# Kernel tuning notes

Hardware: AMD Instinct MI355X
Metric: run time of the kernel (lower is better)

Reference implementation:

```python
import jax, jax.numpy as jnp
import numpy as np

R = 100        # voxel grid resolution per axis
N = 200000     # number of active (non-empty) voxels
K = 3          # kernel size
CIN = 64
COUT = 64
NOFF = K ** 3 - 1  # 26 non-center offsets


def _build_maps():
    # Mirrors mapping_cuda: per kernel offset, find (input_row, output_row) pairs
    # such that coords[input] == coords[output] + offset (submanifold conv,
    # output coords == input coords).
    rng = np.random.default_rng(0)
    lin = rng.choice(R ** 3, size=N, replace=False)
    coords = np.stack(np.unravel_index(lin, (R, R, R)), axis=1)  # [N,3]
    lut = np.full(R ** 3, -1, dtype=np.int64)
    lut[lin] = np.arange(N)
    offs = [(dx, dy, dz) for dx in (-1, 0, 1) for dy in (-1, 0, 1)
            for dz in (-1, 0, 1) if (dx, dy, dz) != (0, 0, 0)]
    ins, outs = [], []
    for d in offs:
        tgt = coords - np.asarray(d)              # output coord receiving input i
        valid = np.all((tgt >= 0) & (tgt < R), axis=1)
        idx_i = np.nonzero(valid)[0]
        tlin = np.ravel_multi_index(tgt[valid].T, (R, R, R))
        j = lut[tlin]
        hit = j >= 0
        ins.append(idx_i[hit].astype(np.int32))
        outs.append(j[hit].astype(np.int32))
    P = max(len(a) for a in ins)
    imap = np.full((NOFF, P), -1, dtype=np.int32)
    omap = np.full((NOFF, P), -1, dtype=np.int32)
    for k, (a, b) in enumerate(zip(ins, outs)):
        imap[k, :len(a)] = a
        omap[k, :len(b)] = b
    return jnp.asarray(imap), jnp.asarray(omap)


def setup_inputs() -> dict:
    key = jax.random.key(0)
    kf, kw = jax.random.split(key)
    feats = jax.random.normal(kf, (N, CIN), dtype=jnp.float32)
    # reset_parameters: uniform(-stdv, stdv), stdv = 1/sqrt(out_channels * K^3)
    stdv = 1.0 / float(np.sqrt(COUT * K ** 3))
    kernel = jax.random.uniform(kw, (K ** 3, CIN, COUT), dtype=jnp.float32,
                                minval=-stdv, maxval=stdv)
    imap, omap = _build_maps()
    return {"feats": feats, "kernel": kernel, "imap": imap, "omap": omap}


def reference(feats, kernel, imap, omap):
    # Submanifold sparse 3D conv: gather -> per-offset GEMM -> scatter-add.
    K3 = kernel.shape[0]
    c = K3 // 2  # center offset: identity neighbor map
    w_nc = jnp.concatenate([kernel[:c], kernel[c + 1:]], axis=0)  # [26,Cin,Cout]
    mask = imap >= 0                                   # [26,P]
    gath = feats[jnp.where(mask, imap, 0)] * mask[..., None]   # [26,P,Cin]
    y = jnp.einsum('kpc,kco->kpo', gath, w_nc)         # [26,P,Cout]
    out = feats @ kernel[c]                            # center contribution [N,Cout]
    oi = jnp.where(mask, omap, 0).reshape(-1)          # masked rows add zeros at row 0
    out = out.at[oi].add(y.reshape(-1, y.shape[-1]))
    return out
```

## Files before the change

### kernel.cpp

```cpp
#include <hip/hip_runtime.h>


#define CIN 64
#define COUT 64
#define TR 32
#define NOFF 26

typedef short bf16x8 __attribute__((ext_vector_type(8)));
typedef unsigned short ushort8 __attribute__((ext_vector_type(8)));
typedef float f32x4 __attribute__((ext_vector_type(4)));

__device__ inline unsigned short bfbits(float f) {
    unsigned u = __builtin_bit_cast(unsigned, f);
    u += 0x7fffu + ((u >> 16) & 1u);
    return (unsigned short)(u >> 16);
}

__device__ inline constexpr int kk_of_item(int i) {
    return (i >= 26) ? 13 : 26 - (i < 13 ? i : i + 1);
}

__global__ __launch_bounds__(256) void prep_feats(const float* __restrict__ f,
                                                  unsigned short* __restrict__ fb,
                                                  int n) {
    const int i8 = (blockIdx.x * 256 + threadIdx.x) * 8;
    if (i8 >= n) return;
    const float4 v0 = *(const float4*)(f + i8);
    const float4 v1 = *(const float4*)(f + i8 + 4);
    union { unsigned short u[8]; bf16x8 v; } r;
    r.u[0] = bfbits(v0.x); r.u[1] = bfbits(v0.y);
    r.u[2] = bfbits(v0.z); r.u[3] = bfbits(v0.w);
    r.u[4] = bfbits(v1.x); r.u[5] = bfbits(v1.y);
    r.u[6] = bfbits(v1.z); r.u[7] = bfbits(v1.w);
    *(bf16x8*)(fb + i8) = r.v;
}

__global__ __launch_bounds__(256) void prep_wt(const float* __restrict__ W,
                                               unsigned short* __restrict__ Wt) {
    const int k = blockIdx.x;
    for (int idx = threadIdx.x; idx < CIN * COUT; idx += 256) {
        const int c = idx >> 6, o = idx & 63;
        const int q = c >> 3, e = c & 7;
        Wt[((k * 64 + o) * 64) + (((q ^ (o & 7)) << 3) + e)] =
            bfbits(W[(k * 64 + c) * 64 + o]);
    }
}

__global__ __launch_bounds__(256) void prep_tab_init(int* __restrict__ tab,
                                                     int nt, int N) {
    const size_t i4 = ((size_t)blockIdx.x * 256 + threadIdx.x) * 4;
    const size_t total = (size_t)27 * nt * TR;
    if (i4 >= total) return;
    const size_t mstep = (size_t)nt * TR;
    int4 v;
    int* vp = (int*)&v;
#pragma unroll
    for (int e = 0; e < 4; ++e) {
        const size_t l = i4 + e;
        const int m = (int)(l / mstep);
        const int r = (int)(l - (size_t)m * mstep);
        vp[e] = (m == 26 && r < N) ? r : N;
    }
    *(int4*)(tab + i4) = v;
}

__global__ __launch_bounds__(256) void prep_tab(const int* __restrict__ imap,
                                                const int* __restrict__ omap,
                                                int P, int nt,
                                                int* __restrict__ tab) {
    const int p = blockIdx.x * 256 + threadIdx.x;
    const int m = blockIdx.y;
    if (p >= P) return;
    const int iv = imap[(size_t)m * P + p];
    if (iv < 0) return;
    tab[((size_t)m * nt + (iv >> 5)) * TR + (iv & 31)] = omap[(size_t)m * P + p];
}

__global__ __launch_bounds__(256, 4) void spconv_v8(
    const unsigned short* __restrict__ fb,
    const unsigned short* __restrict__ wt,
    const int* __restrict__ tab,
    float* __restrict__ out, int N, int nt, int nwg)
{
    __shared__ unsigned short wbuf[2][4096];

    const int tid = threadIdx.x, w = tid >> 6, lane = tid & 63;
    const int col = lane & 15, grp = lane >> 4;

    const int orig = blockIdx.x;
    const int q = nwg >> 3, r8 = nwg & 7;
    const int xcd = orig & 7, kb = orig >> 3;
    const int sb = (xcd < r8 ? xcd * (q + 1) : r8 * (q + 1) + (xcd - r8) * q) + kb;

    const int t = sb * 4 + w;
    const int tt = (t < nt) ? t : (nt - 1);
    const int r0 = t * TR;
    const size_t tstep = (size_t)nt * TR;
    const int* tb = tab + (size_t)tt * TR + col;

    int svr[27][2];
    bf16x8 af[27][2][2];
    ushort8 wr[27][2];

#pragma unroll
    for (int j = 0; j < 4; ++j)
#pragma unroll
        for (int s = 0; s < 2; ++s) svr[j][s] = tb[(size_t)j * tstep + s * 16];

#pragma unroll
    for (int j = 0; j < 2; ++j)
#pragma unroll
        for (int s = 0; s < 2; ++s) {
            const bf16x8* fp = (const bf16x8*)(fb + (size_t)svr[j][s] * 64 + grp * 8);
            af[j][s][0] = fp[0];
            af[j][s][1] = fp[4];
        }

    {
        const unsigned short* wk0 = wt + kk_of_item(0) * 4096;
        const ushort8 t0 = *(const ushort8*)(wk0 + tid * 8);
        const ushort8 t1 = *(const ushort8*)(wk0 + 2048 + tid * 8);
        const unsigned short* wk1 = wt + kk_of_item(1) * 4096;
        wr[1][0] = *(const ushort8*)(wk1 + tid * 8);
        wr[1][1] = *(const ushort8*)(wk1 + 2048 + tid * 8);
        *(ushort8*)(&wbuf[0][tid * 8]) = t0;
        *(ushort8*)(&wbuf[0][2048 + tid * 8]) = t1;
    }
    asm volatile("s_waitcnt lgkmcnt(0)" ::: "memory");
    __builtin_amdgcn_s_barrier();

    f32x4 acc[2][4];
#pragma unroll
    for (int s = 0; s < 2; ++s)
#pragma unroll
        for (int ot = 0; ot < 4; ++ot) acc[s][ot] = {0.f, 0.f, 0.f, 0.f};

#pragma unroll
    for (int it = 0; it < 27; ++it) {
        if (it + 2 <= 26) {
            const unsigned short* wk = wt + kk_of_item(it + 2) * 4096;
            wr[it + 2][0] = *(const ushort8*)(wk + tid * 8);
            wr[it + 2][1] = *(const ushort8*)(wk + 2048 + tid * 8);
        }
        if (it + 2 <= 26) {
#pragma unroll
            for (int s = 0; s < 2; ++s) {
                const bf16x8* fp = (const bf16x8*)(fb + (size_t)svr[it + 2][s] * 64 + grp * 8);
                af[it + 2][s][0] = fp[0];
                af[it + 2][s][1] = fp[4];
            }
        }
        if (it + 4 <= 26) {
#pragma unroll
            for (int s = 0; s < 2; ++s)
                svr[it + 4][s] = tb[(size_t)(it + 4) * tstep + s * 16];
        }
        if (it + 1 <= 26) {
            unsigned short* nb = wbuf[(it + 1) & 1];
            *(ushort8*)(&nb[tid * 8]) = wr[it + 1][0];
            *(ushort8*)(&nb[2048 + tid * 8]) = wr[it + 1][1];
        }
        const unsigned short* cb = wbuf[it & 1];
        __builtin_amdgcn_s_setprio(1);
#pragma unroll
        for (int ot = 0; ot < 4; ++ot) {
            const int o = ot * 16 + col;
            const bf16x8 b0 = *(const bf16x8*)(cb + o * 64 + ((grp ^ (col & 7)) << 3));
            const bf16x8 b1 = *(const bf16x8*)(cb + o * 64 + (((4 + grp) ^ (col & 7)) << 3));
#pragma unroll
            for (int s = 0; s < 2; ++s) {
                acc[s][ot] = __builtin_amdgcn_mfma_f32_16x16x32_bf16(af[it][s][0], b0, acc[s][ot], 0, 0, 0);
                acc[s][ot] = __builtin_amdgcn_mfma_f32_16x16x32_bf16(af[it][s][1], b1, acc[s][ot], 0, 0, 0);
            }
        }
        __builtin_amdgcn_s_setprio(0);
        if (it < 26) {
            asm volatile("s_waitcnt lgkmcnt(0)" ::: "memory");
            __builtin_amdgcn_s_barrier();
        }
    }

#pragma unroll
    for (int s = 0; s < 2; ++s)
#pragma unroll
        for (int ot = 0; ot < 4; ++ot) {
            const f32x4 cv = acc[s][ot];
#pragma unroll
            for (int reg = 0; reg < 4; ++reg) {
                const int rr = r0 + s * 16 + grp * 4 + reg;
                if (rr < N) out[(size_t)rr * 64 + ot * 16 + col] = cv[reg];
            }
        }
}

template <int MODE>
__global__ __launch_bounds__(256) void spconv_fb(
    const float* __restrict__ feats, const float* __restrict__ W,
    const int* __restrict__ imap, const int* __restrict__ omap,
    float* __restrict__ out, int npairs)
{
    __shared__ float4 wt4[16 * 64];
    const int tid = threadIdx.x, koff = blockIdx.y;
    const float* Wk;
    const int* im = nullptr; const int* om = nullptr;
    if (MODE == 0) Wk = W + 13 * (CIN * COUT);
    else {
        const int kk = (koff < 13) ? koff : koff + 1;
        Wk = W + (size_t)kk * (CIN * COUT);
        im = imap + (size_t)koff * npairs; om = omap + (size_t)koff * npairs;
    }
    float* wts = (float*)wt4;
    for (int idx = tid; idx < CIN * COUT; idx += 256) {
        const int c = idx >> 6, o = idx & 63;
        wts[((c >> 2) * 64 + o) * 4 + (c & 3)] = Wk[idx];
    }
    __syncthreads();
    const int o = tid & 63, w = tid >> 6;
    const int base = blockIdx.x * 256 + w * 64;
    const float4* f4p = (const float4*)feats;
    for (int n = 0; n < 64; ++n) {
        const int p = base + n;
        if (p >= npairs) break;
        int i, j;
        if (MODE == 0) { i = p; j = p; }
        else { i = im[p]; if (i < 0) continue; j = om[p]; }
        i = __builtin_amdgcn_readfirstlane(i);
        float a = 0.f;
#pragma unroll
        for (int c4 = 0; c4 < 16; ++c4) {
            const float4 f = f4p[(size_t)i * 16 + c4];
            const float4 wv = wt4[c4 * 64 + o];
            a += f.x * wv.x + f.y * wv.y + f.z * wv.z + f.w * wv.w;
        }
        if (MODE == 0) out[(size_t)j * COUT + o] = a;
        else atomicAdd(&out[(size_t)j * COUT + o], a);
    }
}

extern "C" void kernel_launch(void* const* d_in, const int* in_sizes, int n_in,
                              void* d_out, int out_size, void* d_ws, size_t ws_size,
                              hipStream_t stream) {
    const float* feats = (const float*)d_in[0];
    const float* W     = (const float*)d_in[1];
    const int* imap    = (const int*)d_in[2];
    const int* omap    = (const int*)d_in[3];
    float* out         = (float*)d_out;

    const int N = in_sizes[0] / CIN;
    const int P = in_sizes[2] / NOFF;
    const int nt = (N + TR - 1) / TR;

    const size_t fb_bytes  = (size_t)(N + 1) * 64 * sizeof(unsigned short);
    const size_t wt_bytes  = 27 * 64 * 64 * sizeof(unsigned short);
    const size_t tab_bytes = (size_t)27 * nt * TR * sizeof(int);

    if (ws_size < fb_bytes + wt_bytes + tab_bytes) {
        dim3 blk(256);
        dim3 gc((N + 255) / 256, 1);
        spconv_fb<0><<<gc, blk, 0, stream>>>(feats, W, nullptr, nullptr, out, N);
        dim3 go((P + 255) / 256, NOFF);
        spconv_fb<1><<<go, blk, 0, stream>>>(feats, W, imap, omap, out, P);
        return;
    }

    unsigned short* fbp = (unsigned short*)d_ws;
    unsigned short* Wt  = (unsigned short*)((char*)d_ws + fb_bytes);
    int* tab            = (int*)((char*)d_ws + fb_bytes + wt_bytes);

    const int nf = N * 64;
    prep_feats<<<(nf / 8 + 255) / 256, 256, 0, stream>>>(feats, fbp, nf);
    hipMemsetAsync(fbp + (size_t)N * 64, 0, 128, stream);
    prep_wt<<<27, 256, 0, stream>>>(W, Wt);
    const size_t tot4 = (size_t)27 * nt * TR / 4;
    prep_tab_init<<<(int)((tot4 + 255) / 256), 256, 0, stream>>>(tab, nt, N);
    prep_tab<<<dim3((P + 255) / 256, NOFF), 256, 0, stream>>>(imap, omap, P, nt, tab);

    const int nwg = (nt + 3) / 4;
    spconv_v8<<<nwg, 256, 0, stream>>>(fbp, Wt, tab, out, N, nt, nwg);
}
```

Before: 98.13 us.

## Use 64-row tiles with 2-wave blocks and async global-to-LDS weight pipeline

```diff
diff --git a/kernel.cpp b/kernel.cpp
--- a/kernel.cpp
+++ b/kernel.cpp
@@ -3,11 +3,11 @@
 
 #define CIN 64
 #define COUT 64
-#define TR 32
+#define TR 64
 #define NOFF 26
+#define NSLOT 3
 
 typedef short bf16x8 __attribute__((ext_vector_type(8)));
-typedef unsigned short ushort8 __attribute__((ext_vector_type(8)));
 typedef float f32x4 __attribute__((ext_vector_type(4)));
 
 __device__ inline unsigned short bfbits(float f) {
@@ -22,16 +22,20 @@
 
 __global__ __launch_bounds__(256) void prep_feats(const float* __restrict__ f,
                                                   unsigned short* __restrict__ fb,
-                                                  int n) {
+                                                  int n, int next) {
     const int i8 = (blockIdx.x * 256 + threadIdx.x) * 8;
-    if (i8 >= n) return;
-    const float4 v0 = *(const float4*)(f + i8);
-    const float4 v1 = *(const float4*)(f + i8 + 4);
+    if (i8 >= next) return;
     union { unsigned short u[8]; bf16x8 v; } r;
-    r.u[0] = bfbits(v0.x); r.u[1] = bfbits(v0.y);
-    r.u[2] = bfbits(v0.z); r.u[3] = bfbits(v0.w);
-    r.u[4] = bfbits(v1.x); r.u[5] = bfbits(v1.y);
-    r.u[6] = bfbits(v1.z); r.u[7] = bfbits(v1.w);
+    if (i8 >= n) {
+        r.v = (bf16x8)0;
+    } else {
+        const float4 v0 = *(const float4*)(f + i8);
+        const float4 v1 = *(const float4*)(f + i8 + 4);
+        r.u[0] = bfbits(v0.x); r.u[1] = bfbits(v0.y);
+        r.u[2] = bfbits(v0.z); r.u[3] = bfbits(v0.w);
+        r.u[4] = bfbits(v1.x); r.u[5] = bfbits(v1.y);
+        r.u[6] = bfbits(v1.z); r.u[7] = bfbits(v1.w);
+    }
     *(bf16x8*)(fb + i8) = r.v;
 }
 
@@ -49,17 +53,19 @@
 __global__ __launch_bounds__(256) void prep_tab_init(int* __restrict__ tab,
                                                      int nt, int N) {
     const size_t i4 = ((size_t)blockIdx.x * 256 + threadIdx.x) * 4;
-    const size_t total = (size_t)27 * nt * TR;
+    const size_t total = (size_t)27 * nt * 64;
     if (i4 >= total) return;
-    const size_t mstep = (size_t)nt * TR;
-    int4 v;
-    int* vp = (int*)&v;
+    const size_t mstep = (size_t)nt * 64;
+    int4 v; int* vp = (int*)&v;
 #pragma unroll
     for (int e = 0; e < 4; ++e) {
         const size_t l = i4 + e;
         const int m = (int)(l / mstep);
-        const int r = (int)(l - (size_t)m * mstep);
-        vp[e] = (m == 26 && r < N) ? r : N;
+        const size_t rem = l - (size_t)m * mstep;
+        const int tile = (int)(rem >> 6);
+        const int ee = (int)(rem & 63);
+        const int row = tile * 64 + (ee & 3) * 16 + (ee >> 2);
+        vp[e] = (m == 26 && row < N) ? row : N;
     }
     *(int4*)(tab + i4) = v;
 }
@@ -73,16 +79,18 @@
     if (p >= P) return;
     const int iv = imap[(size_t)m * P + p];
     if (iv < 0) return;
-    tab[((size_t)m * nt + (iv >> 5)) * TR + (iv & 31)] = omap[(size_t)m * P + p];
-}
-
-__global__ __launch_bounds__(256, 4) void spconv_v8(
+    const int tile = iv >> 6, rowin = iv & 63;
+    tab[((size_t)m * nt + tile) * 64 + (rowin & 15) * 4 + (rowin >> 4)] =
+        omap[(size_t)m * P + p];
+}
+
+__global__ __launch_bounds__(128, 2) void spconv_v9(
     const unsigned short* __restrict__ fb,
     const unsigned short* __restrict__ wt,
     const int* __restrict__ tab,
     float* __restrict__ out, int N, int nt, int nwg)
 {
-    __shared__ unsigned short wbuf[2][4096];
+    __shared__ unsigned short wbuf[NSLOT][4096];
 
     const int tid = threadIdx.x, w = tid >> 6, lane = tid & 63;
     const int col = lane & 15, grp = lane >> 4;
@@ -92,96 +100,90 @@
     const int xcd = orig & 7, kb = orig >> 3;
     const int sb = (xcd < r8 ? xcd * (q + 1) : r8 * (q + 1) + (xcd - r8) * q) + kb;
 
-    const int t = sb * 4 + w;
+    const int t = sb * 2 + w;
     const int tt = (t < nt) ? t : (nt - 1);
     const int r0 = t * TR;
-    const size_t tstep = (size_t)nt * TR;
-    const int* tb = tab + (size_t)tt * TR + col;
-
-    int svr[27][2];
-    bf16x8 af[27][2][2];
-    ushort8 wr[27][2];
-
-#pragma unroll
-    for (int j = 0; j < 4; ++j)
-#pragma unroll
-        for (int s = 0; s < 2; ++s) svr[j][s] = tb[(size_t)j * tstep + s * 16];
-
-#pragma unroll
-    for (int j = 0; j < 2; ++j)
-#pragma unroll
-        for (int s = 0; s < 2; ++s) {
-            const bf16x8* fp = (const bf16x8*)(fb + (size_t)svr[j][s] * 64 + grp * 8);
-            af[j][s][0] = fp[0];
-            af[j][s][1] = fp[4];
-        }
-
-    {
-        const unsigned short* wk0 = wt + kk_of_item(0) * 4096;
-        const ushort8 t0 = *(const ushort8*)(wk0 + tid * 8);
-        const ushort8 t1 = *(const ushort8*)(wk0 + 2048 + tid * 8);
-        const unsigned short* wk1 = wt + kk_of_item(1) * 4096;
-        wr[1][0] = *(const ushort8*)(wk1 + tid * 8);
-        wr[1][1] = *(const ushort8*)(wk1 + 2048 + tid * 8);
-        *(ushort8*)(&wbuf[0][tid * 8]) = t0;
-        *(ushort8*)(&wbuf[0][2048 + tid * 8]) = t1;
-    }
+
+    int4 svr[27];
+    bf16x8 af[27][4][2];
+    bf16x8 fr[27][8];
+
+    auto tabload = [&](int j) {
+        svr[j] = *(const int4*)(tab + ((size_t)j * nt + tt) * 64 + col * 4);
+    };
+    auto stage = [&](int item) {
+        const unsigned short* wk = wt + kk_of_item(item) * 4096;
+        unsigned short* dst = &wbuf[item % NSLOT][0];
+#pragma unroll
+        for (int qq = 0; qq < 4; ++qq) {
+            const int eoff = (qq * 2 + w) * 512;
+            __builtin_amdgcn_global_load_lds(
+                (const __attribute__((address_space(1))) void*)(wk + eoff + lane * 8),
+                (__attribute__((address_space(3))) void*)(dst + eoff),
+                16, 0, 0);
+        }
+    };
+    auto read_frags = [&](int item) {
+        const unsigned short* cb = &wbuf[item % NSLOT][0];
+#pragma unroll
+        for (int ot = 0; ot < 4; ++ot) {
+            const int o = ot * 16 + col;
+            fr[item][ot * 2 + 0] = *(const bf16x8*)(cb + o * 64 + ((grp ^ (col & 7)) << 3));
+            fr[item][ot * 2 + 1] = *(const bf16x8*)(cb + o * 64 + (((4 + grp) ^ (col & 7)) << 3));
+        }
+    };
+    auto gather = [&](int item) {
+        const int* sv = (const int*)&svr[item];
+#pragma unroll
+        for (int s = 0; s < 4; ++s) {
+            const bf16x8* fp = (const bf16x8*)(fb + (size_t)sv[s] * 64 + grp * 8);
+            af[item][s][0] = fp[0];
+            af[item][s][1] = fp[4];
+        }
+    };
+
+    f32x4 acc[4][4];
+#pragma unroll
+    for (int s = 0; s < 4; ++s)
+#pragma unroll
+        for (int ot = 0; ot < 4; ++ot) acc[s][ot] = {0.f, 0.f, 0.f, 0.f};
+
+    tabload(0); tabload(1); tabload(2);
+    stage(0); stage(1);
+    __builtin_amdgcn_sched_barrier(0);
+    gather(0);
+    asm volatile("s_waitcnt vmcnt(8)" ::: "memory");
     asm volatile("s_waitcnt lgkmcnt(0)" ::: "memory");
     __builtin_amdgcn_s_barrier();
-
-    f32x4 acc[2][4];
-#pragma unroll
-    for (int s = 0; s < 2; ++s)
-#pragma unroll
-        for (int ot = 0; ot < 4; ++ot) acc[s][ot] = {0.f, 0.f, 0.f, 0.f};
+    read_frags(0);
 
 #pragma unroll
     for (int it = 0; it < 27; ++it) {
-        if (it + 2 <= 26) {
-            const unsigned short* wk = wt + kk_of_item(it + 2) * 4096;
-            wr[it + 2][0] = *(const ushort8*)(wk + tid * 8);
-            wr[it + 2][1] = *(const ushort8*)(wk + 2048 + tid * 8);
-        }
-        if (it + 2 <= 26) {
-#pragma unroll
-            for (int s = 0; s < 2; ++s) {
-                const bf16x8* fp = (const bf16x8*)(fb + (size_t)svr[it + 2][s] * 64 + grp * 8);
-                af[it + 2][s][0] = fp[0];
-                af[it + 2][s][1] = fp[4];
-            }
-        }
-        if (it + 4 <= 26) {
-#pragma unroll
-            for (int s = 0; s < 2; ++s)
-                svr[it + 4][s] = tb[(size_t)(it + 4) * tstep + s * 16];
-        }
-        if (it + 1 <= 26) {
-            unsigned short* nb = wbuf[(it + 1) & 1];
-            *(ushort8*)(&nb[tid * 8]) = wr[it + 1][0];
-            *(ushort8*)(&nb[2048 + tid * 8]) = wr[it + 1][1];
-        }
-        const unsigned short* cb = wbuf[it & 1];
-        __builtin_amdgcn_s_setprio(1);
-#pragma unroll
-        for (int ot = 0; ot < 4; ++ot) {
-            const int o = ot * 16 + col;
-            const bf16x8 b0 = *(const bf16x8*)(cb + o * 64 + ((grp ^ (col & 7)) << 3));
-            const bf16x8 b1 = *(const bf16x8*)(cb + o * 64 + (((4 + grp) ^ (col & 7)) << 3));
-#pragma unroll
-            for (int s = 0; s < 2; ++s) {
-                acc[s][ot] = __builtin_amdgcn_mfma_f32_16x16x32_bf16(af[it][s][0], b0, acc[s][ot], 0, 0, 0);
-                acc[s][ot] = __builtin_amdgcn_mfma_f32_16x16x32_bf16(af[it][s][1], b1, acc[s][ot], 0, 0, 0);
-            }
-        }
-        __builtin_amdgcn_s_setprio(0);
-        if (it < 26) {
+        if (it > 0) {
+            if (it <= 24) asm volatile("s_waitcnt vmcnt(9)" ::: "memory");
+            else          asm volatile("s_waitcnt vmcnt(8)" ::: "memory");
             asm volatile("s_waitcnt lgkmcnt(0)" ::: "memory");
             __builtin_amdgcn_s_barrier();
         }
-    }
-
-#pragma unroll
-    for (int s = 0; s < 2; ++s)
+        if (it + 1 <= 26) read_frags(it + 1);
+        if (it + 2 <= 26) stage(it + 2);
+        __builtin_amdgcn_sched_barrier(0);
+        if (it + 1 <= 26) gather(it + 1);
+        if (it + 3 <= 26) tabload(it + 3);
+
+        __builtin_amdgcn_s_setprio(1);
+#pragma unroll
+        for (int ot = 0; ot < 4; ++ot)
+#pragma unroll
+            for (int s = 0; s < 4; ++s) {
+                acc[s][ot] = __builtin_amdgcn_mfma_f32_16x16x32_bf16(af[it][s][0], fr[it][ot * 2 + 0], acc[s][ot], 0, 0, 0);
+                acc[s][ot] = __builtin_amdgcn_mfma_f32_16x16x32_bf16(af[it][s][1], fr[it][ot * 2 + 1], acc[s][ot], 0, 0, 0);
+            }
+        __builtin_amdgcn_s_setprio(0);
+    }
+
+#pragma unroll
+    for (int s = 0; s < 4; ++s)
 #pragma unroll
         for (int ot = 0; ot < 4; ++ot) {
             const f32x4 cv = acc[s][ot];
@@ -252,7 +254,7 @@
 
     const size_t fb_bytes  = (size_t)(N + 1) * 64 * sizeof(unsigned short);
     const size_t wt_bytes  = 27 * 64 * 64 * sizeof(unsigned short);
-    const size_t tab_bytes = (size_t)27 * nt * TR * sizeof(int);
+    const size_t tab_bytes = (size_t)27 * nt * 64 * sizeof(int);
 
     if (ws_size < fb_bytes + wt_bytes + tab_bytes) {
         dim3 blk(256);
@@ -267,14 +269,13 @@
     unsigned short* Wt  = (unsigned short*)((char*)d_ws + fb_bytes);
     int* tab            = (int*)((char*)d_ws + fb_bytes + wt_bytes);
 
-    const int nf = N * 64;
-    prep_feats<<<(nf / 8 + 255) / 256, 256, 0, stream>>>(feats, fbp, nf);
-    hipMemsetAsync(fbp + (size_t)N * 64, 0, 128, stream);
+    const int nf = N * 64, nfe = (N + 1) * 64;
+    prep_feats<<<(nfe / 8 + 255) / 256, 256, 0, stream>>>(feats, fbp, nf, nfe);
     prep_wt<<<27, 256, 0, stream>>>(W, Wt);
-    const size_t tot4 = (size_t)27 * nt * TR / 4;
+    const size_t tot4 = (size_t)27 * nt * 64 / 4;
     prep_tab_init<<<(int)((tot4 + 255) / 256), 256, 0, stream>>>(tab, nt, N);
     prep_tab<<<dim3((P + 255) / 256, NOFF), 256, 0, stream>>>(imap, omap, P, nt, tab);
 
-    const int nwg = (nt + 3) / 4;
-    spconv_v8<<<nwg, 256, 0, stream>>>(fbp, Wt, tab, out, N, nt, nwg);
-}
+    const int nwg = (nt + 1) / 2;
+    spconv_v9<<<nwg, 128, 0, stream>>>(fbp, Wt, tab, out, N, nt, nwg);
+}
```

Measured after the change: 104.5 us. +6.5%, slower.

## Replace dense neighbor table with binary-searched map ranges and fuse prep kernels

Applied to the files above, without the earlier changes.

```diff
diff --git a/kernel.cpp b/kernel.cpp
--- a/kernel.cpp
+++ b/kernel.cpp
@@ -20,69 +20,64 @@
     return (i >= 26) ? 13 : 26 - (i < 13 ? i : i + 1);
 }
 
-__global__ __launch_bounds__(256) void prep_feats(const float* __restrict__ f,
-                                                  unsigned short* __restrict__ fb,
-                                                  int n) {
-    const int i8 = (blockIdx.x * 256 + threadIdx.x) * 8;
-    if (i8 >= n) return;
-    const float4 v0 = *(const float4*)(f + i8);
-    const float4 v1 = *(const float4*)(f + i8 + 4);
-    union { unsigned short u[8]; bf16x8 v; } r;
-    r.u[0] = bfbits(v0.x); r.u[1] = bfbits(v0.y);
-    r.u[2] = bfbits(v0.z); r.u[3] = bfbits(v0.w);
-    r.u[4] = bfbits(v1.x); r.u[5] = bfbits(v1.y);
-    r.u[6] = bfbits(v1.z); r.u[7] = bfbits(v1.w);
-    *(bf16x8*)(fb + i8) = r.v;
-}
-
-__global__ __launch_bounds__(256) void prep_wt(const float* __restrict__ W,
-                                               unsigned short* __restrict__ Wt) {
-    const int k = blockIdx.x;
-    for (int idx = threadIdx.x; idx < CIN * COUT; idx += 256) {
-        const int c = idx >> 6, o = idx & 63;
-        const int q = c >> 3, e = c & 7;
-        Wt[((k * 64 + o) * 64) + (((q ^ (o & 7)) << 3) + e)] =
-            bfbits(W[(k * 64 + c) * 64 + o]);
-    }
-}
-
-__global__ __launch_bounds__(256) void prep_tab_init(int* __restrict__ tab,
-                                                     int nt, int N) {
-    const size_t i4 = ((size_t)blockIdx.x * 256 + threadIdx.x) * 4;
-    const size_t total = (size_t)27 * nt * TR;
-    if (i4 >= total) return;
-    const size_t mstep = (size_t)nt * TR;
-    int4 v;
-    int* vp = (int*)&v;
-#pragma unroll
-    for (int e = 0; e < 4; ++e) {
-        const size_t l = i4 + e;
-        const int m = (int)(l / mstep);
-        const int r = (int)(l - (size_t)m * mstep);
-        vp[e] = (m == 26 && r < N) ? r : N;
-    }
-    *(int4*)(tab + i4) = v;
-}
-
-__global__ __launch_bounds__(256) void prep_tab(const int* __restrict__ imap,
-                                                const int* __restrict__ omap,
-                                                int P, int nt,
-                                                int* __restrict__ tab) {
-    const int p = blockIdx.x * 256 + threadIdx.x;
-    const int m = blockIdx.y;
-    if (p >= P) return;
-    const int iv = imap[(size_t)m * P + p];
-    if (iv < 0) return;
-    tab[((size_t)m * nt + (iv >> 5)) * TR + (iv & 31)] = omap[(size_t)m * P + p];
-}
-
-__global__ __launch_bounds__(256, 4) void spconv_v8(
+__global__ __launch_bounds__(256) void prep_all(
+    const float* __restrict__ feats, unsigned short* __restrict__ fb,
+    const float* __restrict__ W, unsigned short* __restrict__ Wt,
+    const int* __restrict__ imap, int* __restrict__ rg,
+    int N, int P, int nt, int FB)
+{
+    const int bid = blockIdx.x, tid = threadIdx.x;
+    if (bid < FB) {
+        const int i8 = (bid * 256 + tid) * 8;
+        const int nf = N * 64;
+        if (i8 >= (N + 1) * 64) return;
+        union { unsigned short u[8]; bf16x8 v; } r;
+        if (i8 >= nf) {
+            r.v = (bf16x8)0;
+        } else {
+            const float4 v0 = *(const float4*)(feats + i8);
+            const float4 v1 = *(const float4*)(feats + i8 + 4);
+            r.u[0] = bfbits(v0.x); r.u[1] = bfbits(v0.y);
+            r.u[2] = bfbits(v0.z); r.u[3] = bfbits(v0.w);
+            r.u[4] = bfbits(v1.x); r.u[5] = bfbits(v1.y);
+            r.u[6] = bfbits(v1.z); r.u[7] = bfbits(v1.w);
+        }
+        *(bf16x8*)(fb + i8) = r.v;
+    } else if (bid < FB + 27) {
+        const int k = bid - FB;
+        for (int idx = tid; idx < CIN * COUT; idx += 256) {
+            const int c = idx >> 6, o = idx & 63;
+            const int q = c >> 3, e = c & 7;
+            Wt[((k * 64 + o) * 64) + (((q ^ (o & 7)) << 3) + e)] =
+                bfbits(W[(k * 64 + c) * 64 + o]);
+        }
+    } else {
+        const int idx = (bid - FB - 27) * 256 + tid;
+        const int nt1 = nt + 1;
+        if (idx >= NOFF * nt1) return;
+        const int m = idx / nt1, tile = idx % nt1;
+        const int* a = imap + (size_t)m * P;
+        const int target = tile * TR;
+        int lo = 0, hi = P;
+        while (lo < hi) {
+            const int mid = (lo + hi) >> 1;
+            const int v = a[mid];
+            const int key = (v < 0) ? 0x7fffffff : v;
+            if (key < target) lo = mid + 1; else hi = mid;
+        }
+        rg[(size_t)m * nt1 + tile] = lo;
+    }
+}
+
+__global__ __launch_bounds__(256, 4) void spconv_v10(
     const unsigned short* __restrict__ fb,
     const unsigned short* __restrict__ wt,
-    const int* __restrict__ tab,
-    float* __restrict__ out, int N, int nt, int nwg)
+    const int* __restrict__ imap, const int* __restrict__ omap,
+    const int* __restrict__ rg,
+    float* __restrict__ out, int N, int P, int nt, int nwg)
 {
     __shared__ unsigned short wbuf[2][4096];
+    __shared__ int srctab[4][3][32];
 
     const int tid = threadIdx.x, w = tid >> 6, lane = tid & 63;
     const int col = lane & 15, grp = lane >> 4;
@@ -95,26 +90,57 @@
     const int t = sb * 4 + w;
     const int tt = (t < nt) ? t : (nt - 1);
     const int r0 = t * TR;
-    const size_t tstep = (size_t)nt * TR;
-    const int* tb = tab + (size_t)tt * TR + col;
-
-    int svr[27][2];
+    const int nt1 = nt + 1;
+
+    int p0a[27], cnta[27];
+    int mva[27];
     bf16x8 af[27][2][2];
     ushort8 wr[27][2];
 
-#pragma unroll
-    for (int j = 0; j < 4; ++j)
-#pragma unroll
-        for (int s = 0; s < 2; ++s) svr[j][s] = tb[(size_t)j * tstep + s * 16];
-
-#pragma unroll
-    for (int j = 0; j < 2; ++j)
-#pragma unroll
-        for (int s = 0; s < 2; ++s) {
-            const bf16x8* fp = (const bf16x8*)(fb + (size_t)svr[j][s] * 64 + grp * 8);
-            af[j][s][0] = fp[0];
-            af[j][s][1] = fp[4];
-        }
+    auto RGLOAD = [&](int j) {
+        const int* rp = rg + (size_t)j * nt1 + tt;
+        p0a[j] = rp[0];
+        cnta[j] = rp[1];
+    };
+    auto MAPS = [&](int j) {
+        const int p0 = p0a[j];
+        const int cnt = cnta[j] - p0;
+        cnta[j] = cnt;
+        int idx = p0 + ((lane < cnt) ? lane : 0);
+        idx = (idx < P) ? idx : P - 1;
+        const int iv = imap[(size_t)j * P + idx];
+        const int ov = omap[(size_t)j * P + idx];
+        mva[j] = (ov << 6) | ((iv - r0) & 63);
+    };
+    auto STWRITE = [&](int j) {
+        int* st = srctab[w][j % 3];
+        if (lane < 32) st[lane] = N;
+        if (lane < cnta[j]) st[mva[j] & 63] = mva[j] >> 6;
+    };
+    auto READGATHER = [&](int j) {
+        int s0, s1;
+        if (j < 26) {
+            const int* st = srctab[w][j % 3];
+            s0 = st[col];
+            s1 = st[col + 16];
+        } else {
+            const int ra = r0 + col, rb = r0 + 16 + col;
+            s0 = (ra < N) ? ra : N;
+            s1 = (rb < N) ? rb : N;
+        }
+        const bf16x8* fp = (const bf16x8*)(fb + (size_t)s0 * 64 + grp * 8);
+        af[j][0][0] = fp[0];
+        af[j][0][1] = fp[4];
+        const bf16x8* fq = (const bf16x8*)(fb + (size_t)s1 * 64 + grp * 8);
+        af[j][1][0] = fq[0];
+        af[j][1][1] = fq[4];
+    };
+
+#pragma unroll
+    for (int j = 0; j < 4; ++j) if (j < 26) RGLOAD(j);
+#pragma unroll
+    for (int j = 0; j < 3; ++j) if (j < 26) MAPS(j);
+    STWRITE(0); STWRITE(1);
 
     {
         const unsigned short* wk0 = wt + kk_of_item(0) * 4096;
@@ -126,6 +152,7 @@
         *(ushort8*)(&wbuf[0][tid * 8]) = t0;
         *(ushort8*)(&wbuf[0][2048 + tid * 8]) = t1;
     }
+    READGATHER(0);
     asm volatile("s_waitcnt lgkmcnt(0)" ::: "memory");
     __builtin_amdgcn_s_barrier();
 
@@ -137,23 +164,14 @@
 
 #pragma unroll
     for (int it = 0; it < 27; ++it) {
+        if (it + 4 < 26) RGLOAD(it + 4);
+        if (it + 3 < 26) MAPS(it + 3);
+        if (it + 2 < 26) STWRITE(it + 2);
+        if (it + 1 <= 26) READGATHER(it + 1);
         if (it + 2 <= 26) {
             const unsigned short* wk = wt + kk_of_item(it + 2) * 4096;
             wr[it + 2][0] = *(const ushort8*)(wk + tid * 8);
             wr[it + 2][1] = *(const ushort8*)(wk + 2048 + tid * 8);
-        }
-        if (it + 2 <= 26) {
-#pragma unroll
-            for (int s = 0; s < 2; ++s) {
-                const bf16x8* fp = (const bf16x8*)(fb + (size_t)svr[it + 2][s] * 64 + grp * 8);
-                af[it + 2][s][0] = fp[0];
-                af[it + 2][s][1] = fp[4];
-            }
-        }
-        if (it + 4 <= 26) {
-#pragma unroll
-            for (int s = 0; s < 2; ++s)
-                svr[it + 4][s] = tb[(size_t)(it + 4) * tstep + s * 16];
         }
         if (it + 1 <= 26) {
             unsigned short* nb = wbuf[(it + 1) & 1];
@@ -249,12 +267,13 @@
     const int N = in_sizes[0] / CIN;
     const int P = in_sizes[2] / NOFF;
     const int nt = (N + TR - 1) / TR;
-
-    const size_t fb_bytes  = (size_t)(N + 1) * 64 * sizeof(unsigned short);
-    const size_t wt_bytes  = 27 * 64 * 64 * sizeof(unsigned short);
-    const size_t tab_bytes = (size_t)27 * nt * TR * sizeof(int);
-
-    if (ws_size < fb_bytes + wt_bytes + tab_bytes) {
+    const int nt1 = nt + 1;
+
+    const size_t fb_bytes = (size_t)(N + 1) * 64 * sizeof(unsigned short);
+    const size_t wt_bytes = 27 * 64 * 64 * sizeof(unsigned short);
+    const size_t rg_bytes = (size_t)NOFF * nt1 * sizeof(int);
+
+    if (ws_size < fb_bytes + wt_bytes + rg_bytes) {
         dim3 blk(256);
         dim3 gc((N + 255) / 256, 1);
         spconv_fb<0><<<gc, blk, 0, stream>>>(feats, W, nullptr, nullptr, out, N);
@@ -265,16 +284,14 @@
 
     unsigned short* fbp = (unsigned short*)d_ws;
     unsigned short* Wt  = (unsigned short*)((char*)d_ws + fb_bytes);
-    int* tab            = (int*)((char*)d_ws + fb_bytes + wt_bytes);
-
-    const int nf = N * 64;
-    prep_feats<<<(nf / 8 + 255) / 256, 256, 0, stream>>>(feats, fbp, nf);
-    hipMemsetAsync(fbp + (size_t)N * 64, 0, 128, stream);
-    prep_wt<<<27, 256, 0, stream>>>(W, Wt);
-    const size_t tot4 = (size_t)27 * nt * TR / 4;
-    prep_tab_init<<<(int)((tot4 + 255) / 256), 256, 0, stream>>>(tab, nt, N);
-    prep_tab<<<dim3((P + 255) / 256, NOFF), 256, 0, stream>>>(imap, omap, P, nt, tab);
+    int* rg             = (int*)((char*)d_ws + fb_bytes + wt_bytes);
+
+    const int FB  = ((N + 1) * 64 + 2047) / 2048;
+    const int RGB = (NOFF * nt1 + 255) / 256;
+    prep_all<<<FB + 27 + RGB, 256, 0, stream>>>(feats, fbp, W, Wt, imap, rg,
+                                                N, P, nt, FB);
 
     const int nwg = (nt + 3) / 4;
-    spconv_v8<<<nwg, 256, 0, stream>>>(fbp, Wt, tab, out, N, nt, nwg);
-}
+    spconv_v10<<<nwg, 256, 0, stream>>>(fbp, Wt, imap, omap, rg, out,
+                                        N, P, nt, nwg);
+}
```

Measured after the change: 88.21 us. -10.1%, faster.

## Stage gathers and weights via direct global-to-LDS loads with triple buffering

Applied to the files above, without the earlier changes.

```diff
diff --git a/kernel.cpp b/kernel.cpp
--- a/kernel.cpp
+++ b/kernel.cpp
@@ -7,7 +7,6 @@
 #define NOFF 26
 
 typedef short bf16x8 __attribute__((ext_vector_type(8)));
-typedef unsigned short ushort8 __attribute__((ext_vector_type(8)));
 typedef float f32x4 __attribute__((ext_vector_type(4)));
 
 __device__ inline unsigned short bfbits(float f) {
@@ -20,69 +19,78 @@
     return (i >= 26) ? 13 : 26 - (i < 13 ? i : i + 1);
 }
 
-__global__ __launch_bounds__(256) void prep_feats(const float* __restrict__ f,
-                                                  unsigned short* __restrict__ fb,
-                                                  int n) {
-    const int i8 = (blockIdx.x * 256 + threadIdx.x) * 8;
-    if (i8 >= n) return;
-    const float4 v0 = *(const float4*)(f + i8);
-    const float4 v1 = *(const float4*)(f + i8 + 4);
-    union { unsigned short u[8]; bf16x8 v; } r;
-    r.u[0] = bfbits(v0.x); r.u[1] = bfbits(v0.y);
-    r.u[2] = bfbits(v0.z); r.u[3] = bfbits(v0.w);
-    r.u[4] = bfbits(v1.x); r.u[5] = bfbits(v1.y);
-    r.u[6] = bfbits(v1.z); r.u[7] = bfbits(v1.w);
-    *(bf16x8*)(fb + i8) = r.v;
-}
-
-__global__ __launch_bounds__(256) void prep_wt(const float* __restrict__ W,
-                                               unsigned short* __restrict__ Wt) {
-    const int k = blockIdx.x;
-    for (int idx = threadIdx.x; idx < CIN * COUT; idx += 256) {
-        const int c = idx >> 6, o = idx & 63;
-        const int q = c >> 3, e = c & 7;
-        Wt[((k * 64 + o) * 64) + (((q ^ (o & 7)) << 3) + e)] =
-            bfbits(W[(k * 64 + c) * 64 + o]);
-    }
-}
-
-__global__ __launch_bounds__(256) void prep_tab_init(int* __restrict__ tab,
-                                                     int nt, int N) {
-    const size_t i4 = ((size_t)blockIdx.x * 256 + threadIdx.x) * 4;
-    const size_t total = (size_t)27 * nt * TR;
-    if (i4 >= total) return;
-    const size_t mstep = (size_t)nt * TR;
-    int4 v;
-    int* vp = (int*)&v;
-#pragma unroll
-    for (int e = 0; e < 4; ++e) {
-        const size_t l = i4 + e;
-        const int m = (int)(l / mstep);
-        const int r = (int)(l - (size_t)m * mstep);
-        vp[e] = (m == 26 && r < N) ? r : N;
-    }
-    *(int4*)(tab + i4) = v;
-}
-
-__global__ __launch_bounds__(256) void prep_tab(const int* __restrict__ imap,
-                                                const int* __restrict__ omap,
-                                                int P, int nt,
-                                                int* __restrict__ tab) {
+__global__ __launch_bounds__(256) void prep_all(
+    const float* __restrict__ feats, unsigned short* __restrict__ fb,
+    const float* __restrict__ W, unsigned short* __restrict__ Wt,
+    int4* __restrict__ tab4, int N, int nt, int FB)
+{
+    const int bid = blockIdx.x, tid = threadIdx.x;
+    if (bid < FB) {
+        const int i8 = (bid * 256 + tid) * 8;
+        const int nf = N * 64;
+        if (i8 >= (N + 1) * 64) return;
+        union { unsigned short u[8]; bf16x8 v; } r;
+        if (i8 >= nf) {
+            r.v = (bf16x8)0;
+        } else {
+            const float4 v0 = *(const float4*)(feats + i8);
+            const float4 v1 = *(const float4*)(feats + i8 + 4);
+            r.u[0] = bfbits(v0.x); r.u[1] = bfbits(v0.y);
+            r.u[2] = bfbits(v0.z); r.u[3] = bfbits(v0.w);
+            r.u[4] = bfbits(v1.x); r.u[5] = bfbits(v1.y);
+            r.u[6] = bfbits(v1.z); r.u[7] = bfbits(v1.w);
+        }
+        *(bf16x8*)(fb + i8) = r.v;
+    } else if (bid < FB + 27) {
+        const int k = bid - FB;
+        for (int idx = tid; idx < CIN * COUT; idx += 256) {
+            const int c = idx >> 6, o = idx & 63;
+            const int q = c >> 3, e = c & 7;
+            Wt[((k * 64 + o) * 64) + (((q ^ (o & 7)) << 3) + e)] =
+                bfbits(W[(k * 64 + c) * 64 + o]);
+        }
+    } else {
+        const long long idx4 = (long long)(bid - FB - 27) * 256 + tid;
+        const long long tot4 = (long long)27 * nt * 8;
+        if (idx4 >= tot4) return;
+        const int m = (int)(idx4 / ((long long)nt * 8));
+        const long long rem = idx4 - (long long)m * nt * 8;
+        const int tile = (int)(rem >> 3), k = (int)(rem & 7);
+        int4 v;
+        if (m == 26) {
+            const int b = tile * 32 + k;
+            v.x = (b      < N) ? b      : N;
+            v.y = (b + 8  < N) ? b + 8  : N;
+            v.z = (b + 16 < N) ? b + 16 : N;
+            v.w = (b + 24 < N) ? b + 24 : N;
+        } else {
+            v = make_int4(N, N, N, N);
+        }
+        tab4[idx4] = v;
+    }
+}
+
+__global__ __launch_bounds__(256) void prep_scatter(
+    const int* __restrict__ imap, const int* __restrict__ omap,
+    int P, int nt, int* __restrict__ tabi)
+{
     const int p = blockIdx.x * 256 + threadIdx.x;
     const int m = blockIdx.y;
     if (p >= P) return;
     const int iv = imap[(size_t)m * P + p];
     if (iv < 0) return;
-    tab[((size_t)m * nt + (iv >> 5)) * TR + (iv & 31)] = omap[(size_t)m * P + p];
-}
-
-__global__ __launch_bounds__(256, 4) void spconv_v8(
+    const int ov = omap[(size_t)m * P + p];
+    tabi[(((size_t)m * nt + (iv >> 5)) * 8 + (iv & 7)) * 4 + ((iv >> 3) & 3)] = ov;
+}
+
+__global__ __launch_bounds__(256, 2) void spconv_v14(
     const unsigned short* __restrict__ fb,
     const unsigned short* __restrict__ wt,
-    const int* __restrict__ tab,
+    const int4* __restrict__ tab,
     float* __restrict__ out, int N, int nt, int nwg)
 {
-    __shared__ unsigned short wbuf[2][4096];
+    __shared__ unsigned short wbuf[3][4096];
+    __shared__ unsigned short gbuf[4][3][2048];
 
     const int tid = threadIdx.x, w = tid >> 6, lane = tid & 63;
     const int col = lane & 15, grp = lane >> 4;
@@ -95,38 +103,52 @@
     const int t = sb * 4 + w;
     const int tt = (t < nt) ? t : (nt - 1);
     const int r0 = t * TR;
-    const size_t tstep = (size_t)nt * TR;
-    const int* tb = tab + (size_t)tt * TR + col;
-
-    int svr[27][2];
-    bf16x8 af[27][2][2];
-    ushort8 wr[27][2];
-
-#pragma unroll
-    for (int j = 0; j < 4; ++j)
-#pragma unroll
-        for (int s = 0; s < 2; ++s) svr[j][s] = tb[(size_t)j * tstep + s * 16];
-
-#pragma unroll
-    for (int j = 0; j < 2; ++j)
-#pragma unroll
-        for (int s = 0; s < 2; ++s) {
-            const bf16x8* fp = (const bf16x8*)(fb + (size_t)svr[j][s] * 64 + grp * 8);
-            af[j][s][0] = fp[0];
-            af[j][s][1] = fp[4];
-        }
-
-    {
-        const unsigned short* wk0 = wt + kk_of_item(0) * 4096;
-        const ushort8 t0 = *(const ushort8*)(wk0 + tid * 8);
-        const ushort8 t1 = *(const ushort8*)(wk0 + 2048 + tid * 8);
-        const unsigned short* wk1 = wt + kk_of_item(1) * 4096;
-        wr[1][0] = *(const ushort8*)(wk1 + tid * 8);
-        wr[1][1] = *(const ushort8*)(wk1 + 2048 + tid * 8);
-        *(ushort8*)(&wbuf[0][tid * 8]) = t0;
-        *(ushort8*)(&wbuf[0][2048 + tid * 8]) = t1;
-    }
-    asm volatile("s_waitcnt lgkmcnt(0)" ::: "memory");
+
+    int4 svr[27];
+    const size_t tbase = (size_t)tt * 8 + (lane >> 3);
+    const size_t tstep = (size_t)nt * 8;
+
+    auto TAB = [&](int j) {
+        if (j <= 26) {
+            svr[j] = tab[(size_t)j * tstep + tbase];
+        } else {
+            int4 d = tab[(size_t)26 * tstep + tbase];
+            asm volatile("" :: "v"(d.x), "v"(d.y), "v"(d.z), "v"(d.w));
+        }
+    };
+    auto WSTAGE = [&](int item) {
+        const int ic = (item <= 26) ? item : 26;
+        const unsigned short* wk = wt + kk_of_item(ic) * 4096;
+        unsigned short* dst = &wbuf[item % 3][0];
+#pragma unroll
+        for (int c = 0; c < 2; ++c) {
+            const int ch = (c * 4 + w) * 512;
+            __builtin_amdgcn_global_load_lds(
+                (const __attribute__((address_space(1))) void*)(wk + ch + lane * 8),
+                (__attribute__((address_space(3))) void*)(dst + ch), 16, 0, 0);
+        }
+    };
+    const int swg = (((lane & 7) ^ ((lane >> 3) & 7)) << 3);
+    auto GATHER = [&](int item) {
+        const int ic = (item <= 26) ? item : 26;
+        const int4 s4 = svr[ic];
+        unsigned short* dst = &gbuf[w][item % 3][0];
+#pragma unroll
+        for (int c = 0; c < 4; ++c) {
+            const int row = (c == 0) ? s4.x : (c == 1) ? s4.y : (c == 2) ? s4.z : s4.w;
+            __builtin_amdgcn_global_load_lds(
+                (const __attribute__((address_space(1))) void*)(fb + (size_t)row * 64 + swg),
+                (__attribute__((address_space(3))) void*)(dst + c * 512), 16, 0, 0);
+        }
+    };
+
+#pragma unroll
+    for (int j = 0; j < 6; ++j) TAB(j);
+    WSTAGE(0); WSTAGE(1);
+    __builtin_amdgcn_sched_barrier(0);
+    GATHER(0); GATHER(1); GATHER(2);
+    __builtin_amdgcn_sched_barrier(0);
+    asm volatile("s_waitcnt vmcnt(12)" ::: "memory");
     __builtin_amdgcn_s_barrier();
 
     f32x4 acc[2][4];
@@ -137,45 +159,46 @@
 
 #pragma unroll
     for (int it = 0; it < 27; ++it) {
-        if (it + 2 <= 26) {
-            const unsigned short* wk = wt + kk_of_item(it + 2) * 4096;
-            wr[it + 2][0] = *(const ushort8*)(wk + tid * 8);
-            wr[it + 2][1] = *(const ushort8*)(wk + 2048 + tid * 8);
-        }
-        if (it + 2 <= 26) {
+        TAB(it + 6);
+        __builtin_amdgcn_sched_barrier(0);
+        if (it == 0)      asm volatile("s_waitcnt vmcnt(9)"  ::: "memory");
+        else if (it == 1) asm volatile("s_waitcnt vmcnt(12)" ::: "memory");
+        else              asm volatile("s_waitcnt vmcnt(15)" ::: "memory");
+        __builtin_amdgcn_sched_barrier(0);
+        bf16x8 a[2][2], b[8];
+        {
+            const unsigned short* gb = &gbuf[w][it % 3][0];
 #pragma unroll
             for (int s = 0; s < 2; ++s) {
-                const bf16x8* fp = (const bf16x8*)(fb + (size_t)svr[it + 2][s] * 64 + grp * 8);
-                af[it + 2][s][0] = fp[0];
-                af[it + 2][s][1] = fp[4];
+                const int row = col + s * 16;
+#pragma unroll
+                for (int h = 0; h < 2; ++h)
+                    a[s][h] = *(const bf16x8*)(gb + row * 64 + (((h * 4 + grp) ^ (col & 7)) << 3));
             }
-        }
-        if (it + 4 <= 26) {
-#pragma unroll
-            for (int s = 0; s < 2; ++s)
-                svr[it + 4][s] = tb[(size_t)(it + 4) * tstep + s * 16];
-        }
-        if (it + 1 <= 26) {
-            unsigned short* nb = wbuf[(it + 1) & 1];
-            *(ushort8*)(&nb[tid * 8]) = wr[it + 1][0];
-            *(ushort8*)(&nb[2048 + tid * 8]) = wr[it + 1][1];
-        }
-        const unsigned short* cb = wbuf[it & 1];
+            const unsigned short* wb = &wbuf[it % 3][0];
+#pragma unroll
+            for (int ot = 0; ot < 4; ++ot)
+#pragma unroll
+                for (int h = 0; h < 2; ++h)
+                    b[ot * 2 + h] = *(const bf16x8*)(wb + (ot * 16 + col) * 64 + (((h * 4 + grp) ^ (col & 7)) << 3));
+        }
+        asm volatile("s_waitcnt lgkmcnt(0)" ::: "memory");
+        __builtin_amdgcn_sched_barrier(0);
+        WSTAGE(it + 2);
+        __builtin_amdgcn_sched_barrier(0);
+        GATHER(it + 3);
+        __builtin_amdgcn_sched_barrier(0);
         __builtin_amdgcn_s_setprio(1);
 #pragma unroll
-        for (int ot = 0; ot < 4; ++ot) {
-            const int o = ot * 16 + col;
-            const bf16x8 b0 = *(const bf16x8*)(cb + o * 64 + ((grp ^ (col & 7)) << 3));
-            const bf16x8 b1 = *(const bf16x8*)(cb + o * 64 + (((4 + grp) ^ (col & 7)) << 3));
+        for (int ot = 0; ot < 4; ++ot)
 #pragma unroll
             for (int s = 0; s < 2; ++s) {
-                acc[s][ot] = __builtin_amdgcn_mfma_f32_16x16x32_bf16(af[it][s][0], b0, acc[s][ot], 0, 0, 0);
-                acc[s][ot] = __builtin_amdgcn_mfma_f32_16x16x32_bf16(af[it][s][1], b1, acc[s][ot], 0, 0, 0);
+                acc[s][ot] = __builtin_amdgcn_mfma_f32_16x16x32_bf16(a[s][0], b[ot * 2 + 0], acc[s][ot], 0, 0, 0);
+                acc[s][ot] = __builtin_amdgcn_mfma_f32_16x16x32_bf16(a[s][1], b[ot * 2 + 1], acc[s][ot], 0, 0, 0);
             }
-        }
         __builtin_amdgcn_s_setprio(0);
         if (it < 26) {
-            asm volatile("s_waitcnt lgkmcnt(0)" ::: "memory");
+            asm volatile("s_waitcnt vmcnt(11)" ::: "memory");
             __builtin_amdgcn_s_barrier();
         }
     }
@@ -252,7 +275,7 @@
 
     const size_t fb_bytes  = (size_t)(N + 1) * 64 * sizeof(unsigned short);
     const size_t wt_bytes  = 27 * 64 * 64 * sizeof(unsigned short);
-    const size_t tab_bytes = (size_t)27 * nt * TR * sizeof(int);
+    const size_t tab_bytes = (size_t)27 * nt * 8 * sizeof(int4);
 
     if (ws_size < fb_bytes + wt_bytes + tab_bytes) {
         dim3 blk(256);
@@ -265,16 +288,14 @@
 
     unsigned short* fbp = (unsigned short*)d_ws;
     unsigned short* Wt  = (unsigned short*)((char*)d_ws + fb_bytes);
-    int* tab            = (int*)((char*)d_ws + fb_bytes + wt_bytes);
-
-    const int nf = N * 64;
-    prep_feats<<<(nf / 8 + 255) / 256, 256, 0, stream>>>(feats, fbp, nf);
-    hipMemsetAsync(fbp + (size_t)N * 64, 0, 128, stream);
-    prep_wt<<<27, 256, 0, stream>>>(W, Wt);
-    const size_t tot4 = (size_t)27 * nt * TR / 4;
-    prep_tab_init<<<(int)((tot4 + 255) / 256), 256, 0, stream>>>(tab, nt, N);
-    prep_tab<<<dim3((P + 255) / 256, NOFF), 256, 0, stream>>>(imap, omap, P, nt, tab);
+    int4* tab           = (int4*)((char*)d_ws + fb_bytes + wt_bytes);
+
+    const int FB = ((N + 1) * 64 + 2047) / 2048;
+    const long long tot4 = (long long)27 * nt * 8;
+    const int TI = (int)((tot4 + 255) / 256);
+    prep_all<<<FB + 27 + TI, 256, 0, stream>>>(feats, fbp, W, Wt, tab, N, nt, FB);
+    prep_scatter<<<dim3((P + 255) / 256, NOFF), 256, 0, stream>>>(imap, omap, P, nt, (int*)tab);
 
     const int nwg = (nt + 3) / 4;
-    spconv_v8<<<nwg, 256, 0, stream>>>(fbp, Wt, tab, out, N, nt, nwg);
-}
+    spconv_v14<<<nwg, 256, 0, stream>>>(fbp, Wt, tab, out, N, nt, nwg);
+}
```

Result: slower. 102.8 us (+4.8%).
